# Optimization experiments

Measured on AMD Instinct MI355X. Metric: run time of the kernel, lower is better.

Reference implementation:

```python
import jax, jax.numpy as jnp
import numpy as np

B, S, H, NH = 2, 2048, 1024, 16
HD = H // NH


def setup_inputs() -> dict:
    key = jax.random.key(0)
    ks = jax.random.split(key, 12)
    query = jax.random.normal(ks[0], (B, S, H), dtype=jnp.float32)
    key_t = jax.random.normal(ks[1], (B, S, H), dtype=jnp.float32)
    value = jax.random.normal(ks[2], (B, S, H), dtype=jnp.float32)
    kpm = jax.random.randint(ks[3], (B, S), 0, 2).astype(bool)
    kpm = kpm.at[:, 0].set(False)  # guarantee at least one unmasked key per row
    bias = jax.random.normal(ks[4], (1, NH, S, S), dtype=jnp.float32)
    init = 0.02
    q_w = jax.random.normal(ks[5], (H, H), dtype=jnp.float32) * init
    k_w = jax.random.normal(ks[6], (H, H), dtype=jnp.float32) * init
    v_w = jax.random.normal(ks[7], (H, H), dtype=jnp.float32) * init
    o_w = jax.random.normal(ks[8], (H, H), dtype=jnp.float32) * init
    q_b = jnp.zeros((H,), jnp.float32)
    k_b = jnp.zeros((H,), jnp.float32)
    v_b = jnp.zeros((H,), jnp.float32)
    o_b = jnp.zeros((H,), jnp.float32)
    return {"query": query, "key": key_t, "value": value,
            "key_padding_mask": kpm, "bias": bias,
            "q_w": q_w, "q_b": q_b, "k_w": k_w, "k_b": k_b,
            "v_w": v_w, "v_b": v_b, "o_w": o_w, "o_b": o_b}


def _shape(x):
    # [B, S, H] -> [B, NH, S, HD]
    b, s, _ = x.shape
    return x.reshape(b, s, NH, HD).transpose(0, 2, 1, 3)


def reference(query, key, value, key_padding_mask, bias,
              q_w, q_b, k_w, k_b, v_w, v_b, o_w, o_b):
    scale = HD ** -0.5
    q = _shape(query @ q_w.T + q_b)
    k = _shape(key @ k_w.T + k_b)
    v = _shape(value @ v_w.T + v_b)
    attn = jnp.einsum('bhqd,bhkd->bhqk', q, k) * scale + bias
    mask = key_padding_mask[:, None, None, :]  # [B,1,1,S]
    attn = jnp.where(mask, -jnp.inf, attn)
    probs = jax.nn.softmax(attn, axis=-1)
    # safe-softmax: zero masked entries and renormalize with clamped denom
    probs = jnp.where(mask, 0.0, probs)
    denom = jnp.maximum(probs.sum(axis=-1, keepdims=True), 1e-6)
    probs = probs / denom
    ctx = jnp.einsum('bhqk,bhkd->bhqd', probs, v)
    ctx = ctx.transpose(0, 2, 1, 3).reshape(query.shape[0], query.shape[1], H)
    return ctx @ o_w.T + o_b
```

## Files before the change

### kernel.cpp

```cpp
#include <hip/hip_runtime.h>
#include <math.h>

#define Ss  2048
#define Hh  1024

typedef unsigned short u16;
typedef __attribute__((ext_vector_type(8))) short short8;
typedef __attribute__((ext_vector_type(4))) float fx4;

__device__ __forceinline__ u16 f2bf(float f) {
  unsigned int u = __float_as_uint(f);
  u = (u + 0x7fffu + ((u >> 16) & 1u)) >> 16;
  return (u16)u;
}

__device__ __forceinline__ void gld_lds16(const u16* g, u16* l) {
  __builtin_amdgcn_global_load_lds(
      (const __attribute__((address_space(1))) unsigned int*)(const unsigned int*)g,
      (__attribute__((address_space(3))) unsigned int*)(unsigned int*)l, 16, 0, 0);
}

#define MFMA16(a,b,c) __builtin_amdgcn_mfma_f32_16x16x32_bf16((a),(b),(c),0,0,0)

__global__ __launch_bounds__(256) void cast3(const float* __restrict__ a,
    const float* __restrict__ b, const float* __restrict__ c,
    u16* __restrict__ oa, u16* __restrict__ ob, u16* __restrict__ oc) {
  const int z = blockIdx.z;
  const float* in = z == 0 ? a : (z == 1 ? b : c);
  u16* out = z == 0 ? oa : (z == 1 ? ob : oc);
  const int i = (blockIdx.x * 256 + threadIdx.x) * 4;
  const float4 v = *(const float4*)(in + i);
  ushort4 r; r.x = f2bf(v.x); r.y = f2bf(v.y); r.z = f2bf(v.z); r.w = f2bf(v.w);
  *(ushort4*)(out + i) = r;
}

__global__ __launch_bounds__(256) void cast4(const float* __restrict__ a,
    const float* __restrict__ b, const float* __restrict__ c, const float* __restrict__ d,
    u16* __restrict__ oa, u16* __restrict__ ob, u16* __restrict__ oc, u16* __restrict__ od) {
  const int z = blockIdx.z;
  const float* in = z == 0 ? a : (z == 1 ? b : (z == 2 ? c : d));
  u16* out = z == 0 ? oa : (z == 1 ? ob : (z == 2 ? oc : od));
  const int i = (blockIdx.x * 256 + threadIdx.x) * 4;
  const float4 v = *(const float4*)(in + i);
  ushort4 r; r.x = f2bf(v.x); r.y = f2bf(v.y); r.z = f2bf(v.z); r.w = f2bf(v.w);
  *(ushort4*)(out + i) = r;
}

__global__ __launch_bounds__(256) void build_maskadd(const int* __restrict__ kpm,
                                                     float* __restrict__ ma) {
  const int i = blockIdx.x * 256 + threadIdx.x;
  ma[i] = kpm[i] ? -1.0e30f : 0.0f;
}

template <int MODE>
__device__ __forceinline__ void gemm_core(const u16* __restrict__ A,
    const u16* __restrict__ W, const float* __restrict__ bias,
    void* __restrict__ out, float scale) {
  __shared__ __align__(16) u16 As[4096];
  __shared__ __align__(16) u16 Bs[4096];
  const int tid = threadIdx.x;
  const int w = tid >> 6, lane = tid & 63, ln = lane & 15, quad = lane >> 4;
  const int i0 = blockIdx.y * 128, j0 = blockIdx.x * 128;
  const int wr = (w & 1) * 64, wc = (w >> 1) * 64;
  fx4 acc[4][4] = {};
  const int L0 = w * 64 + lane, L1 = L0 + 256;
  const u16* sa0 = A + (size_t)(i0 + (L0 & 127)) * 1024 + (L0 >> 7) * 8;
  const u16* sa1 = A + (size_t)(i0 + (L1 & 127)) * 1024 + (L1 >> 7) * 8;
  const u16* sb0 = W + (size_t)(j0 + (L0 & 127)) * 1024 + (L0 >> 7) * 8;
  const u16* sb1 = W + (size_t)(j0 + (L1 & 127)) * 1024 + (L1 >> 7) * 8;
  u16* da0 = As + (w * 64) * 8;  u16* da1 = As + (256 + w * 64) * 8;
  u16* db0 = Bs + (w * 64) * 8;  u16* db1 = Bs + (256 + w * 64) * 8;
  for (int k0 = 0; k0 < 1024; k0 += 32) {
    __syncthreads();
    gld_lds16(sa0 + k0, da0); gld_lds16(sa1 + k0, da1);
    gld_lds16(sb0 + k0, db0); gld_lds16(sb1 + k0, db1);
    __syncthreads();
    short8 a[4], b[4];
#pragma unroll
    for (int t = 0; t < 4; ++t) {
      a[t] = *(const short8*)&As[(quad * 128 + wr + t * 16 + ln) * 8];
      b[t] = *(const short8*)&Bs[(quad * 128 + wc + t * 16 + ln) * 8];
    }
#pragma unroll
    for (int mt = 0; mt < 4; ++mt)
#pragma unroll
      for (int nt = 0; nt < 4; ++nt)
        acc[mt][nt] = MFMA16(a[mt], b[nt], acc[mt][nt]);
  }
#pragma unroll
  for (int nt = 0; nt < 4; ++nt) {
    const int col = j0 + wc + nt * 16 + ln;
    const float bv = bias[col];
#pragma unroll
    for (int mt = 0; mt < 4; ++mt)
#pragma unroll
      for (int r = 0; r < 4; ++r) {
        const int row = i0 + wr + mt * 16 + quad * 4 + r;
        const float val = (acc[mt][nt][r] + bv) * scale;
        if (MODE == 1) {
          const int bb = row >> 11, s = row & 2047, h = col >> 6, d = col & 63;
          ((u16*)out)[((size_t)(bb * 16 + h) * 2048 + s) * 64 + d] = f2bf(val);
        } else {
          ((float*)out)[(size_t)row * 1024 + col] = val;
        }
      }
  }
}

__global__ __launch_bounds__(256) void gemm_qkv(
    const u16* xq, const u16* xk, const u16* xv,
    const u16* wq, const u16* wk, const u16* wv,
    const float* bq, const float* bk, const float* bv,
    u16* q, u16* k, u16* v) {
  const int z = blockIdx.z;
  const u16* A = z == 0 ? xq : (z == 1 ? xk : xv);
  const u16* W = z == 0 ? wq : (z == 1 ? wk : wv);
  const float* bb = z == 0 ? bq : (z == 1 ? bk : bv);
  u16* o = z == 0 ? q : (z == 1 ? k : v);
  const float sc = z == 0 ? 0.125f : 1.0f;
  gemm_core<1>(A, W, bb, o, sc);
}

__global__ __launch_bounds__(256) void gemm_o(const u16* ctx, const u16* wo,
                                              const float* ob, float* out) {
  gemm_core<0>(ctx, wo, ob, out, 1.0f);
}

__global__ __launch_bounds__(256) void transpose_v(const u16* __restrict__ v,
                                                   u16* __restrict__ vt) {
  __shared__ u16 T[64][72];
  const int tid = threadIdx.x;
  const int bh = blockIdx.y, s0 = blockIdx.x * 64;
#pragma unroll
  for (int i = 0; i < 2; ++i) {
    const int L = i * 256 + tid, key = L >> 3, dc = L & 7;
    const uint4 val = *(const uint4*)&v[((size_t)bh * 2048 + s0 + key) * 64 + dc * 8];
    *(uint4*)&T[key][dc * 8] = val;
  }
  __syncthreads();
#pragma unroll
  for (int i = 0; i < 2; ++i) {
    const int L = i * 256 + tid, d = L >> 3, kc = L & 7;
    u16 tmp[8];
#pragma unroll
    for (int j = 0; j < 8; ++j) tmp[j] = T[kc * 8 + j][d];
    *(uint4*)&vt[((size_t)bh * 64 + d) * 2048 + s0 + kc * 8] = *(const uint4*)tmp;
  }
}

__global__ __launch_bounds__(256) void attn(const u16* __restrict__ Qb,
    const u16* __restrict__ Kb, const u16* __restrict__ VT,
    const float* __restrict__ bias, const float* __restrict__ maskadd,
    u16* __restrict__ ctx) {
  __shared__ __align__(16) u16 Ks[4096];
  __shared__ __align__(16) u16 Vs[4096];
  __shared__ __align__(16) u16 Ps[4096];
  const int tid = threadIdx.x;
  const int w = tid >> 6, lane = tid & 63, ln = lane & 15, quad = lane >> 4;
  const int q0 = blockIdx.x * 64;
  const int hb = blockIdx.y, h = hb >> 1, b = hb & 1, bh = b * 16 + h;
  const int wr = w * 16;

  short8 qf[2];
#pragma unroll
  for (int ks = 0; ks < 2; ++ks)
    qf[ks] = *(const short8*)&Qb[((size_t)bh * 2048 + q0 + wr + ln) * 64 +
                                 ks * 32 + quad * 8];
  float mi[4], li[4];
  fx4 O[4] = {};
#pragma unroll
  for (int r = 0; r < 4; ++r) { mi[r] = -3.0e38f; li[r] = 0.f; }

  const int L0 = w * 64 + lane, L1 = L0 + 256;
  const u16* sk0 = Kb + ((size_t)bh * 2048 + (L0 & 63)) * 64 + (L0 >> 6) * 8;
  const u16* sk1 = Kb + ((size_t)bh * 2048 + (L1 & 63)) * 64 + (L1 >> 6) * 8;
  const u16* sv0 = VT + ((size_t)bh * 64 + (L0 & 63)) * 2048 + (L0 >> 6) * 8;
  const u16* sv1 = VT + ((size_t)bh * 64 + (L1 & 63)) * 2048 + (L1 >> 6) * 8;
  u16* dk0 = Ks + (w * 64) * 8;  u16* dk1 = Ks + (256 + w * 64) * 8;
  u16* dv0 = Vs + (w * 64) * 8;  u16* dv1 = Vs + (256 + w * 64) * 8;

  const float* bq = bias + (size_t)h * Ss * Ss;
  float bcur[4][4], macur[4];
#pragma unroll
  for (int r = 0; r < 4; ++r) {
    const int qg = q0 + wr + quad * 4 + r;
#pragma unroll
    for (int nt = 0; nt < 4; ++nt)
      bcur[nt][r] = bq[(size_t)qg * Ss + nt * 16 + ln];
  }
#pragma unroll
  for (int nt = 0; nt < 4; ++nt) macur[nt] = maskadd[b * Ss + nt * 16 + ln];

  for (int kt = 0; kt < Ss; kt += 64) {
    __syncthreads();
    gld_lds16(sk0 + (size_t)kt * 64, dk0);
    gld_lds16(sk1 + (size_t)kt * 64, dk1);
    gld_lds16(sv0 + kt, dv0);
    gld_lds16(sv1 + kt, dv1);
    __syncthreads();

    fx4 S[4] = {};
#pragma unroll
    for (int ks = 0; ks < 2; ++ks)
#pragma unroll
      for (int nt = 0; nt < 4; ++nt) {
        const short8 kf = *(const short8*)&Ks[((ks * 4 + quad) * 64 + nt * 16 + ln) * 8];
        S[nt] = MFMA16(qf[ks], kf, S[nt]);
      }

    float alpha[4];
#pragma unroll
    for (int r = 0; r < 4; ++r) {
      const float s0 = S[0][r] + bcur[0][r] + macur[0];
      const float s1 = S[1][r] + bcur[1][r] + macur[1];
      const float s2 = S[2][r] + bcur[2][r] + macur[2];
      const float s3 = S[3][r] + bcur[3][r] + macur[3];
      float mx = fmaxf(fmaxf(s0, s1), fmaxf(s2, s3));
      mx = fmaxf(mx, __shfl_xor(mx, 1)); mx = fmaxf(mx, __shfl_xor(mx, 2));
      mx = fmaxf(mx, __shfl_xor(mx, 4)); mx = fmaxf(mx, __shfl_xor(mx, 8));
      const float mn = fmaxf(mi[r], mx);
      const float a = __expf(mi[r] - mn);
      const float p0 = __expf(s0 - mn), p1 = __expf(s1 - mn);
      const float p2 = __expf(s2 - mn), p3 = __expf(s3 - mn);
      float rs = p0 + p1 + p2 + p3;
      rs += __shfl_xor(rs, 1); rs += __shfl_xor(rs, 2);
      rs += __shfl_xor(rs, 4); rs += __shfl_xor(rs, 8);
      li[r] = li[r] * a + rs;
      mi[r] = mn; alpha[r] = a;
      const int q = wr + quad * 4 + r;
      const int kcb = ln >> 3, jj = ln & 7;
      Ps[((kcb    ) * 64 + q) * 8 + jj] = f2bf(p0);
      Ps[((kcb + 2) * 64 + q) * 8 + jj] = f2bf(p1);
      Ps[((kcb + 4) * 64 + q) * 8 + jj] = f2bf(p2);
      Ps[((kcb + 6) * 64 + q) * 8 + jj] = f2bf(p3);
    }

    const int kn = (kt + 64 < Ss) ? kt + 64 : kt;
    float bnxt[4][4], manxt[4];
#pragma unroll
    for (int r = 0; r < 4; ++r) {
      const int qg = q0 + wr + quad * 4 + r;
#pragma unroll
      for (int nt = 0; nt < 4; ++nt)
        bnxt[nt][r] = bq[(size_t)qg * Ss + kn + nt * 16 + ln];
    }
#pragma unroll
    for (int nt = 0; nt < 4; ++nt) manxt[nt] = maskadd[b * Ss + kn + nt * 16 + ln];

#pragma unroll
    for (int nt = 0; nt < 4; ++nt)
#pragma unroll
      for (int r = 0; r < 4; ++r) O[nt][r] *= alpha[r];

#pragma unroll
    for (int ks = 0; ks < 2; ++ks) {
      const short8 pf = *(const short8*)&Ps[((ks * 4 + quad) * 64 + wr + ln) * 8];
#pragma unroll
      for (int nt = 0; nt < 4; ++nt) {
        const short8 vf = *(const short8*)&Vs[((ks * 4 + quad) * 64 + nt * 16 + ln) * 8];
        O[nt] = MFMA16(pf, vf, O[nt]);
      }
    }

#pragma unroll
    for (int r = 0; r < 4; ++r) {
      macur[r] = manxt[r];
#pragma unroll
      for (int nt = 0; nt < 4; ++nt) bcur[nt][r] = bnxt[nt][r];
    }
  }

#pragma unroll
  for (int r = 0; r < 4; ++r) {
    const float inv = 1.0f / fmaxf(li[r], 1e-6f);
    const int qg = q0 + wr + quad * 4 + r;
#pragma unroll
    for (int nt = 0; nt < 4; ++nt)
      ctx[((size_t)(b * Ss + qg)) * 1024 + h * 64 + nt * 16 + ln] =
          f2bf(O[nt][r] * inv);
  }
}

extern "C" void kernel_launch(void* const* d_in, const int* in_sizes, int n_in,
                              void* d_out, int out_size, void* d_ws, size_t ws_size,
                              hipStream_t stream) {
  const float* query = (const float*)d_in[0];
  const float* key   = (const float*)d_in[1];
  const float* value = (const float*)d_in[2];
  const int*   kpm   = (const int*)d_in[3];
  const float* bias  = (const float*)d_in[4];
  const float* q_w   = (const float*)d_in[5];
  const float* q_b   = (const float*)d_in[6];
  const float* k_w   = (const float*)d_in[7];
  const float* k_b   = (const float*)d_in[8];
  const float* v_w   = (const float*)d_in[9];
  const float* v_b   = (const float*)d_in[10];
  const float* o_w   = (const float*)d_in[11];
  const float* o_b   = (const float*)d_in[12];
  float* out = (float*)d_out;

  char* ws = (char*)d_ws;
  const size_t MB = 1024 * 1024;
  u16* xq = (u16*)(ws + 0 * MB);
  u16* xk = (u16*)(ws + 8 * MB);
  u16* xv = (u16*)(ws + 16 * MB);
  u16* wq = (u16*)(ws + 24 * MB);
  u16* wk = (u16*)(ws + 26 * MB);
  u16* wv = (u16*)(ws + 28 * MB);
  u16* wo = (u16*)(ws + 30 * MB);
  u16* qb = (u16*)(ws + 32 * MB);
  u16* kb = (u16*)(ws + 40 * MB);
  u16* vb = (u16*)(ws + 48 * MB);
  u16* cx = (u16*)(ws + 56 * MB);
  u16* vt = (u16*)(ws + 0 * MB);
  float* ma = (float*)(ws + 8 * MB);

  cast3<<<dim3(4096, 1, 3), 256, 0, stream>>>(query, key, value, xq, xk, xv);
  cast4<<<dim3(1024, 1, 4), 256, 0, stream>>>(q_w, k_w, v_w, o_w, wq, wk, wv, wo);
  gemm_qkv<<<dim3(8, 32, 3), 256, 0, stream>>>(xq, xk, xv, wq, wk, wv,
                                               q_b, k_b, v_b, qb, kb, vb);
  transpose_v<<<dim3(32, 32), 256, 0, stream>>>(vb, vt);
  build_maskadd<<<dim3(16), 256, 0, stream>>>(kpm, ma);
  attn<<<dim3(32, 32), 256, 0, stream>>>(qb, kb, vt, bias, ma, cx);
  gemm_o<<<dim3(8, 32), 256, 0, stream>>>(cx, wo, o_b, out);
}
```

Before: 616.5 us.

## Double-buffer LDS tiles in projection GEMM and attention loops

The LDS staging buffers for the GEMM A/W tiles and the attention K/V tiles become two-slot ping-pong buffers. The loads for the next tile are issued before computing on the current one, so each iteration needs one barrier instead of two. The attention kernel also issues its bias and mask prefetch before the QK MFMAs rather than after the softmax. This aims to hide global-to-LDS load latency behind MFMA work, at the cost of doubling LDS use per block, which may reduce occupancy.

```diff
diff --git a/kernel.cpp b/kernel.cpp
--- a/kernel.cpp
+++ b/kernel.cpp
@@ -56,8 +56,8 @@
 __device__ __forceinline__ void gemm_core(const u16* __restrict__ A,
     const u16* __restrict__ W, const float* __restrict__ bias,
     void* __restrict__ out, float scale) {
-  __shared__ __align__(16) u16 As[4096];
-  __shared__ __align__(16) u16 Bs[4096];
+  __shared__ __align__(16) u16 As[2][4096];
+  __shared__ __align__(16) u16 Bs[2][4096];
   const int tid = threadIdx.x;
   const int w = tid >> 6, lane = tid & 63, ln = lane & 15, quad = lane >> 4;
   const int i0 = blockIdx.y * 128, j0 = blockIdx.x * 128;
@@ -68,24 +68,31 @@
   const u16* sa1 = A + (size_t)(i0 + (L1 & 127)) * 1024 + (L1 >> 7) * 8;
   const u16* sb0 = W + (size_t)(j0 + (L0 & 127)) * 1024 + (L0 >> 7) * 8;
   const u16* sb1 = W + (size_t)(j0 + (L1 & 127)) * 1024 + (L1 >> 7) * 8;
-  u16* da0 = As + (w * 64) * 8;  u16* da1 = As + (256 + w * 64) * 8;
-  u16* db0 = Bs + (w * 64) * 8;  u16* db1 = Bs + (256 + w * 64) * 8;
+  const int d0 = (w * 64) * 8, d1 = (256 + w * 64) * 8;
+
+  gld_lds16(sa0, &As[0][d0]); gld_lds16(sa1, &As[0][d1]);
+  gld_lds16(sb0, &Bs[0][d0]); gld_lds16(sb1, &Bs[0][d1]);
+  __syncthreads();
+
   for (int k0 = 0; k0 < 1024; k0 += 32) {
-    __syncthreads();
-    gld_lds16(sa0 + k0, da0); gld_lds16(sa1 + k0, da1);
-    gld_lds16(sb0 + k0, db0); gld_lds16(sb1 + k0, db1);
-    __syncthreads();
+    const int cur = (k0 >> 5) & 1;
+    if (k0 + 32 < 1024) {
+      const int nb = cur ^ 1;
+      gld_lds16(sa0 + k0 + 32, &As[nb][d0]); gld_lds16(sa1 + k0 + 32, &As[nb][d1]);
+      gld_lds16(sb0 + k0 + 32, &Bs[nb][d0]); gld_lds16(sb1 + k0 + 32, &Bs[nb][d1]);
+    }
     short8 a[4], b[4];
 #pragma unroll
     for (int t = 0; t < 4; ++t) {
-      a[t] = *(const short8*)&As[(quad * 128 + wr + t * 16 + ln) * 8];
-      b[t] = *(const short8*)&Bs[(quad * 128 + wc + t * 16 + ln) * 8];
+      a[t] = *(const short8*)&As[cur][(quad * 128 + wr + t * 16 + ln) * 8];
+      b[t] = *(const short8*)&Bs[cur][(quad * 128 + wc + t * 16 + ln) * 8];
     }
 #pragma unroll
     for (int mt = 0; mt < 4; ++mt)
 #pragma unroll
       for (int nt = 0; nt < 4; ++nt)
         acc[mt][nt] = MFMA16(a[mt], b[nt], acc[mt][nt]);
+    __syncthreads();
   }
 #pragma unroll
   for (int nt = 0; nt < 4; ++nt) {
@@ -152,8 +159,8 @@
     const u16* __restrict__ Kb, const u16* __restrict__ VT,
     const float* __restrict__ bias, const float* __restrict__ maskadd,
     u16* __restrict__ ctx) {
-  __shared__ __align__(16) u16 Ks[4096];
-  __shared__ __align__(16) u16 Vs[4096];
+  __shared__ __align__(16) u16 Ks[2][4096];
+  __shared__ __align__(16) u16 Vs[2][4096];
   __shared__ __align__(16) u16 Ps[4096];
   const int tid = threadIdx.x;
   const int w = tid >> 6, lane = tid & 63, ln = lane & 15, quad = lane >> 4;
@@ -176,10 +183,12 @@
   const u16* sk1 = Kb + ((size_t)bh * 2048 + (L1 & 63)) * 64 + (L1 >> 6) * 8;
   const u16* sv0 = VT + ((size_t)bh * 64 + (L0 & 63)) * 2048 + (L0 >> 6) * 8;
   const u16* sv1 = VT + ((size_t)bh * 64 + (L1 & 63)) * 2048 + (L1 >> 6) * 8;
-  u16* dk0 = Ks + (w * 64) * 8;  u16* dk1 = Ks + (256 + w * 64) * 8;
-  u16* dv0 = Vs + (w * 64) * 8;  u16* dv1 = Vs + (256 + w * 64) * 8;
+  const int d0 = (w * 64) * 8, d1 = (256 + w * 64) * 8;
 
   const float* bq = bias + (size_t)h * Ss * Ss;
+
+  gld_lds16(sk0, &Ks[0][d0]); gld_lds16(sk1, &Ks[0][d1]);
+  gld_lds16(sv0, &Vs[0][d0]); gld_lds16(sv1, &Vs[0][d1]);
   float bcur[4][4], macur[4];
 #pragma unroll
   for (int r = 0; r < 4; ++r) {
@@ -190,21 +199,35 @@
   }
 #pragma unroll
   for (int nt = 0; nt < 4; ++nt) macur[nt] = maskadd[b * Ss + nt * 16 + ln];
+  __syncthreads();
 
   for (int kt = 0; kt < Ss; kt += 64) {
-    __syncthreads();
-    gld_lds16(sk0 + (size_t)kt * 64, dk0);
-    gld_lds16(sk1 + (size_t)kt * 64, dk1);
-    gld_lds16(sv0 + kt, dv0);
-    gld_lds16(sv1 + kt, dv1);
-    __syncthreads();
+    const int cur = (kt >> 6) & 1;
+    if (kt + 64 < Ss) {
+      const int nb = cur ^ 1;
+      gld_lds16(sk0 + (size_t)(kt + 64) * 64, &Ks[nb][d0]);
+      gld_lds16(sk1 + (size_t)(kt + 64) * 64, &Ks[nb][d1]);
+      gld_lds16(sv0 + kt + 64, &Vs[nb][d0]);
+      gld_lds16(sv1 + kt + 64, &Vs[nb][d1]);
+    }
+    const int kn = (kt + 64 < Ss) ? kt + 64 : kt;
+    float bnxt[4][4], manxt[4];
+#pragma unroll
+    for (int r = 0; r < 4; ++r) {
+      const int qg = q0 + wr + quad * 4 + r;
+#pragma unroll
+      for (int nt = 0; nt < 4; ++nt)
+        bnxt[nt][r] = bq[(size_t)qg * Ss + kn + nt * 16 + ln];
+    }
+#pragma unroll
+    for (int nt = 0; nt < 4; ++nt) manxt[nt] = maskadd[b * Ss + kn + nt * 16 + ln];
 
     fx4 S[4] = {};
 #pragma unroll
     for (int ks = 0; ks < 2; ++ks)
 #pragma unroll
       for (int nt = 0; nt < 4; ++nt) {
-        const short8 kf = *(const short8*)&Ks[((ks * 4 + quad) * 64 + nt * 16 + ln) * 8];
+        const short8 kf = *(const short8*)&Ks[cur][((ks * 4 + quad) * 64 + nt * 16 + ln) * 8];
         S[nt] = MFMA16(qf[ks], kf, S[nt]);
       }
 
@@ -235,18 +258,6 @@
       Ps[((kcb + 6) * 64 + q) * 8 + jj] = f2bf(p3);
     }
 
-    const int kn = (kt + 64 < Ss) ? kt + 64 : kt;
-    float bnxt[4][4], manxt[4];
-#pragma unroll
-    for (int r = 0; r < 4; ++r) {
-      const int qg = q0 + wr + quad * 4 + r;
-#pragma unroll
-      for (int nt = 0; nt < 4; ++nt)
-        bnxt[nt][r] = bq[(size_t)qg * Ss + kn + nt * 16 + ln];
-    }
-#pragma unroll
-    for (int nt = 0; nt < 4; ++nt) manxt[nt] = maskadd[b * Ss + kn + nt * 16 + ln];
-
 #pragma unroll
     for (int nt = 0; nt < 4; ++nt)
 #pragma unroll
@@ -257,7 +268,7 @@
       const short8 pf = *(const short8*)&Ps[((ks * 4 + quad) * 64 + wr + ln) * 8];
 #pragma unroll
       for (int nt = 0; nt < 4; ++nt) {
-        const short8 vf = *(const short8*)&Vs[((ks * 4 + quad) * 64 + nt * 16 + ln) * 8];
+        const short8 vf = *(const short8*)&Vs[cur][((ks * 4 + quad) * 64 + nt * 16 + ln) * 8];
         O[nt] = MFMA16(pf, vf, O[nt]);
       }
     }
@@ -268,6 +279,7 @@
 #pragma unroll
       for (int nt = 0; nt < 4; ++nt) bcur[nt][r] = bnxt[nt][r];
     }
+    __syncthreads();
   }
 
 #pragma unroll
```

After: 611.2 us. Within noise of the previous version (-0.9%).
